# Kernel tuning notes

Measured on AMD Instinct MI355X. Metric: run time of the kernel, lower is better.

## Reference

```python
import jax, jax.numpy as jnp
import numpy as np

EMBED_DIM = 1024
NUM_HEADS = 16
PROJ_DIM = EMBED_DIM // NUM_HEADS


def setup_inputs() -> dict:
    key = jax.random.key(0)
    ks = jax.random.split(key, 11)
    B, S, D = 2, 2048, EMBED_DIM
    scale = 1.0 / np.sqrt(D)
    inp = {
        'q': jax.random.normal(ks[0], (B, S, D), jnp.float32),
        'k': jax.random.normal(ks[1], (B, S, D), jnp.float32),
        'v': jax.random.normal(ks[2], (B, S, D), jnp.float32),
        'Wq': jax.random.normal(ks[3], (D, D), jnp.float32) * scale,
        'bq': jnp.zeros((D,), jnp.float32),
        'Wk': jax.random.normal(ks[4], (D, D), jnp.float32) * scale,
        'bk': jnp.zeros((D,), jnp.float32),
        'Wv': jax.random.normal(ks[5], (D, D), jnp.float32) * scale,
        'bv': jnp.zeros((D,), jnp.float32),
        'Wo': jax.random.normal(ks[6], (D, D), jnp.float32) * scale,
        'bo': jnp.zeros((D,), jnp.float32),
        'use_causal_mask': 1,
    }
    return inp


def _split_heads(x, B):
    # [B, S, D] -> [B, H, S, Pd]
    return x.reshape(B, -1, NUM_HEADS, PROJ_DIM).transpose(0, 2, 1, 3)


def reference(q, k, v, Wq, bq, Wk, bk, Wv, bv, Wo, bo, use_causal_mask):
    B, S, D = q.shape
    qh = _split_heads(q @ Wq + bq, B)
    kh = _split_heads(k @ Wk + bk, B)
    vh = _split_heads(v @ Wv + bv, B)
    # scaled dot-product attention; scores [B, H, S, S]
    logits = jnp.einsum('bhqd,bhkd->bhqk', qh, kh) / jnp.sqrt(
        jnp.asarray(PROJ_DIM, jnp.float32))
    if use_causal_mask:
        # faithful to source: logits += log(tril * 1e-9 + 1e-9)
        tril = jnp.tril(jnp.ones((S, S), dtype=logits.dtype))
        logits = logits + jnp.log(tril * 1e-9 + 1e-9)
    attn = jax.nn.softmax(logits, axis=-1)
    out = jnp.einsum('bhqk,bhkd->bhqd', attn, vh)
    out = out.transpose(0, 2, 1, 3).reshape(B, S, D)
    return out @ Wo + bo
```

## Files before the change

### kernel.cpp

```cpp
#include <hip/hip_runtime.h>
#include <hip/hip_bf16.h>
#include <stdint.h>

#define EMBED 1024
#define NH    16
#define PD    64
#define BATCH 2
#define SEQ   2048

typedef unsigned short u16;
typedef __attribute__((ext_vector_type(8))) short bf16x8;
typedef __attribute__((ext_vector_type(4))) float f32x4;

#define WAITALL() __builtin_amdgcn_s_waitcnt(0)

__device__ __forceinline__ float b2f(u16 x) {
  unsigned u = ((unsigned)x) << 16;
  return __builtin_bit_cast(float, u);
}
__device__ __forceinline__ u16 f2b(float x) {
  unsigned u = __builtin_bit_cast(unsigned, x);
  u += 0x7fffu + ((u >> 16) & 1u);
  return (u16)(u >> 16);
}
__device__ __forceinline__ float loadIn(const void* p, size_t i, int isf32) {
  return isf32 ? ((const float*)p)[i] : b2f(((const u16*)p)[i]);
}
__device__ __forceinline__ void async16(const void* g, void* l) {
  __builtin_amdgcn_global_load_lds((const __attribute__((address_space(1))) void*)g,
                                   (__attribute__((address_space(3))) void*)l,
                                   16, 0, 0);
}
__device__ __forceinline__ int swz(int row, int col) {
  return row * 64 + (col ^ ((row & 7) << 3));
}

__global__ void detect(const unsigned* q, int* flag) {
  if (threadIdx.x == 0) {
    int conc = 0;
    for (int i = 0; i < 64; i++) {
      unsigned lo = q[i] & 0xffffu;
      unsigned e = (lo >> 7) & 0xffu;
      if (e >= 110 && e <= 135) conc++;
    }
    *flag = (conc < 32) ? 1 : 0;
  }
}

__global__ __launch_bounds__(256) void conv_qkv(const void* q, const void* k,
                                                const void* v, u16* qb, u16* kb,
                                                u16* vb, const int* flag) {
  const int isf32 = flag[0];
  size_t i = ((size_t)blockIdx.x * 256 + threadIdx.x) * 8;
  const void* src = (blockIdx.y == 0) ? q : (blockIdx.y == 1) ? k : v;
  u16* dst = (blockIdx.y == 0) ? qb : (blockIdx.y == 1) ? kb : vb;
  u16 tmp[8];
  if (isf32) {
    const float* s = (const float*)src + i;
    float4 a = *(const float4*)s;
    float4 b = *(const float4*)(s + 4);
    tmp[0] = f2b(a.x); tmp[1] = f2b(a.y); tmp[2] = f2b(a.z); tmp[3] = f2b(a.w);
    tmp[4] = f2b(b.x); tmp[5] = f2b(b.y); tmp[6] = f2b(b.z); tmp[7] = f2b(b.w);
  } else {
    const uint4 r = *(const uint4*)((const u16*)src + i);
    *(uint4*)tmp = r;
  }
  *(uint4*)(dst + i) = *(uint4*)tmp;
}

__global__ __launch_bounds__(256) void conv_w(const void* Wq, const void* Wk,
                                              const void* Wv, const void* Wo,
                                              u16* out, const int* flag) {
  const int isf32 = flag[0];
  const void* W = (blockIdx.z == 0) ? Wq : (blockIdx.z == 1) ? Wk
                : (blockIdx.z == 2) ? Wv : Wo;
  u16* WT = out + (size_t)blockIdx.z * EMBED * EMBED;
  __shared__ float sh[64][65];
  int r0 = blockIdx.y * 64, c0 = blockIdx.x * 64;
  int col = threadIdx.x & 63;
  int rb  = threadIdx.x >> 6;
#pragma unroll
  for (int i = 0; i < 16; i++) {
    int row = i * 4 + rb;
    sh[row][col] = loadIn(W, (size_t)(r0 + row) * EMBED + c0 + col, isf32);
  }
  __syncthreads();
#pragma unroll
  for (int i = 0; i < 16; i++) {
    int row = i * 4 + rb;
    WT[(size_t)(c0 + row) * EMBED + r0 + col] = f2b(sh[col][row]);
  }
}

__device__ __forceinline__ void gemm_core(const u16* __restrict__ A,
                                          const u16* __restrict__ Bt,
                                          int tm, int tn, u16* lds,
                                          f32x4 acc[4][4]) {
  const int tid = threadIdx.x;
  const int lane = tid & 63;
  const int wv = tid >> 6;
  const int wm = (wv >> 1) * 64, wn = (wv & 1) * 64;
  const int l15 = lane & 15, quad = lane >> 4;
  const int rb = (lane & 7) << 3;
  u16* As = lds;
  u16* Bs = lds + 128 * 64;
  f32x4 z = {0.f, 0.f, 0.f, 0.f};
#pragma unroll
  for (int i = 0; i < 4; i++)
#pragma unroll
    for (int j = 0; j < 4; j++) acc[i][j] = z;

  for (int kt = 0; kt < EMBED; kt += 64) {
#pragma unroll
    for (int i = 0; i < 4; i++) {
      int c = i * 256 + tid;
      int row = c >> 3;
      int col = ((c & 7) << 3) ^ ((row & 7) << 3);
      async16(A + (size_t)(tm + row) * EMBED + kt + col, As + c * 8);
      async16(Bt + (size_t)(tn + row) * EMBED + kt + col, Bs + c * 8);
    }
    WAITALL();
    __syncthreads();
#pragma unroll
    for (int ks = 0; ks < 64; ks += 32) {
      int ko = (ks + quad * 8) ^ rb;
      bf16x8 af[4], bf[4];
#pragma unroll
      for (int mt = 0; mt < 4; mt++)
        af[mt] = *(const bf16x8*)(As + (wm + mt * 16 + l15) * 64 + ko);
#pragma unroll
      for (int nt = 0; nt < 4; nt++)
        bf[nt] = *(const bf16x8*)(Bs + (wn + nt * 16 + l15) * 64 + ko);
#pragma unroll
      for (int mt = 0; mt < 4; mt++)
#pragma unroll
        for (int nt = 0; nt < 4; nt++)
          acc[mt][nt] = __builtin_amdgcn_mfma_f32_16x16x32_bf16(
              af[mt], bf[nt], acc[mt][nt], 0, 0, 0);
    }
    WAITALL();
    __syncthreads();
  }
}

__global__ __launch_bounds__(256) void qkv_gemm(
    const u16* qb, const u16* kb, const u16* vb, const u16* wts,
    const void* bq, const void* bk, const void* bv,
    u16* Qh, u16* Kh, u16* Vt, const int* flag) {
  __shared__ __align__(16) u16 lds[2 * 128 * 64];
  const int isf32 = flag[0];
  int z = blockIdx.z;
  const u16* A = (z == 0) ? qb : (z == 1) ? kb : vb;
  const u16* Bt = wts + (size_t)z * EMBED * EMBED;
  const void* bias = (z == 0) ? bq : (z == 1) ? bk : bv;
  int tm = blockIdx.y * 128, tn = blockIdx.x * 128;
  f32x4 acc[4][4];
  gemm_core(A, Bt, tm, tn, lds, acc);

  int lane = threadIdx.x & 63, wv = threadIdx.x >> 6;
  int wm = (wv >> 1) * 64, wn = (wv & 1) * 64;
  int rbase = tm + wm + ((lane >> 4) << 2);
  int cbase = tn + wn + (lane & 15);
  if (z < 2) {
    u16* dst = (z == 0) ? Qh : Kh;
#pragma unroll
    for (int mt = 0; mt < 4; mt++)
#pragma unroll
      for (int nt = 0; nt < 4; nt++) {
        int col = cbase + nt * 16;
        float bv_ = loadIn(bias, col, isf32);
        int h = col >> 6, p = col & 63;
#pragma unroll
        for (int j = 0; j < 4; j++) {
          int row = rbase + mt * 16 + j;
          int b = row >> 11, s = row & 2047;
          dst[(((size_t)(b * NH + h) * SEQ) + s) * PD + p] =
              f2b(acc[mt][nt][j] + bv_);
        }
      }
  } else {
#pragma unroll
    for (int mt = 0; mt < 4; mt++)
#pragma unroll
      for (int nt = 0; nt < 4; nt++) {
        int col = cbase + nt * 16;
        float bv_ = loadIn(bias, col, isf32);
        int h = col >> 6, p = col & 63;
        int row0 = rbase + mt * 16;
        int b = row0 >> 11, s0 = row0 & 2047;
        ushort4 pk;
        pk.x = f2b(acc[mt][nt][0] + bv_);
        pk.y = f2b(acc[mt][nt][1] + bv_);
        pk.z = f2b(acc[mt][nt][2] + bv_);
        pk.w = f2b(acc[mt][nt][3] + bv_);
        *(ushort4*)(Vt + ((size_t)(b * NH + h) * PD + p) * SEQ + s0) = pk;
      }
  }
}

__global__ __launch_bounds__(256) void attn(const u16* __restrict__ Qh,
                                            const u16* __restrict__ Kh,
                                            const u16* __restrict__ Vt,
                                            u16* __restrict__ O,
                                            const int* __restrict__ maskflag) {
  __shared__ __align__(16) u16 Qs[128 * 64];
  __shared__ __align__(16) u16 Ks[64 * 64];
  __shared__ __align__(16) u16 Vs[64 * 64];
  __shared__ __align__(16) u16 Ps[128 * 64];
  const int bh = blockIdx.y;
  const int qt = blockIdx.x * 128;
  const int tid = threadIdx.x, lane = tid & 63, wv = tid >> 6;
  const int l15 = lane & 15, quad = lane >> 4;
  const int rb = (lane & 7) << 3;
  const size_t head = (size_t)bh * SEQ * PD;
  const bool causal = (maskflag[0] != 0);
  const float C = 0.18033688011112042f;

#pragma unroll
  for (int i = 0; i < 4; i++) {
    int c = i * 256 + tid;
    int row = c >> 3;
    int col = ((c & 7) << 3) ^ ((row & 7) << 3);
    async16(Qh + head + (size_t)(qt + row) * PD + col, Qs + c * 8);
  }

  float lacc[2][4];
  f32x4 oacc[2][4];
  f32x4 z4 = {0.f, 0.f, 0.f, 0.f};
#pragma unroll
  for (int mt = 0; mt < 2; mt++)
#pragma unroll
    for (int j = 0; j < 4; j++) lacc[mt][j] = 0.f;
#pragma unroll
  for (int mt = 0; mt < 2; mt++)
#pragma unroll
    for (int nt = 0; nt < 4; nt++) oacc[mt][nt] = z4;

  const int rowq = qt + wv * 32 + (quad << 2);

  for (int t = 0; t < SEQ / 64; t++) {
    const int k0 = t * 64;
#pragma unroll
    for (int i = 0; i < 2; i++) {
      int c = i * 256 + tid;
      int row = c >> 3;
      int col = ((c & 7) << 3) ^ ((row & 7) << 3);
      async16(Kh + head + (size_t)(k0 + row) * PD + col, Ks + c * 8);
      async16(Vt + head + (size_t)row * SEQ + k0 + col, Vs + c * 8);
    }
    WAITALL();
    __syncthreads();

    f32x4 s[2][4];
#pragma unroll
    for (int mt = 0; mt < 2; mt++)
#pragma unroll
      for (int nt = 0; nt < 4; nt++) s[mt][nt] = z4;
#pragma unroll
    for (int ks = 0; ks < 64; ks += 32) {
      int ko = (ks + quad * 8) ^ rb;
      bf16x8 aq[2];
      aq[0] = *(const bf16x8*)(Qs + (wv * 32 + l15) * 64 + ko);
      aq[1] = *(const bf16x8*)(Qs + (wv * 32 + 16 + l15) * 64 + ko);
#pragma unroll
      for (int nt = 0; nt < 4; nt++) {
        bf16x8 bk8 = *(const bf16x8*)(Ks + (nt * 16 + l15) * 64 + ko);
        s[0][nt] = __builtin_amdgcn_mfma_f32_16x16x32_bf16(aq[0], bk8, s[0][nt], 0, 0, 0);
        s[1][nt] = __builtin_amdgcn_mfma_f32_16x16x32_bf16(aq[1], bk8, s[1][nt], 0, 0, 0);
      }
    }

    const int mode = !causal ? 0 : (k0 > qt + 127 ? 2 : (k0 + 63 <= qt ? 0 : 1));
    const float ub = (mode == 2) ? -17.f : -16.f;
#pragma unroll
    for (int mt = 0; mt < 2; mt++) {
      const int row = rowq + mt * 16;
      const int prow = wv * 32 + mt * 16 + (quad << 2);
#pragma unroll
      for (int nt = 0; nt < 4; nt++) {
        const int col = k0 + nt * 16 + l15;
        const int pcol = nt * 16 + l15;
#pragma unroll
        for (int j = 0; j < 4; j++) {
          float bias = ub;
          if (mode == 1 && col > row + j) bias = -17.f;
          float p = exp2f(fmaf(s[mt][nt][j], C, bias));
          lacc[mt][j] += p;
          Ps[(prow + j) * 64 + (pcol ^ (((prow + j) & 7) << 3))] = f2b(p);
        }
      }
    }

#pragma unroll
    for (int ks = 0; ks < 64; ks += 32) {
      int ko = (ks + quad * 8) ^ rb;
      bf16x8 ap[2];
      ap[0] = *(const bf16x8*)(Ps + (wv * 32 + l15) * 64 + ko);
      ap[1] = *(const bf16x8*)(Ps + (wv * 32 + 16 + l15) * 64 + ko);
#pragma unroll
      for (int nt = 0; nt < 4; nt++) {
        bf16x8 bv8 = *(const bf16x8*)(Vs + (nt * 16 + l15) * 64 + ko);
        oacc[0][nt] = __builtin_amdgcn_mfma_f32_16x16x32_bf16(ap[0], bv8, oacc[0][nt], 0, 0, 0);
        oacc[1][nt] = __builtin_amdgcn_mfma_f32_16x16x32_bf16(ap[1], bv8, oacc[1][nt], 0, 0, 0);
      }
    }
    WAITALL();
    __syncthreads();
  }

#pragma unroll
  for (int off = 1; off < 16; off <<= 1)
#pragma unroll
    for (int mt = 0; mt < 2; mt++)
#pragma unroll
      for (int j = 0; j < 4; j++)
        lacc[mt][j] += __shfl_xor(lacc[mt][j], off, 64);

  const int b = bh >> 4, h = bh & 15;
#pragma unroll
  for (int mt = 0; mt < 2; mt++) {
#pragma unroll
    for (int j = 0; j < 4; j++) {
      float inv = 1.f / lacc[mt][j];
      int qrow = qt + wv * 32 + mt * 16 + (quad << 2) + j;
      size_t base = ((size_t)b * SEQ + qrow) * EMBED + h * PD;
#pragma unroll
      for (int nt = 0; nt < 4; nt++) {
        int p = nt * 16 + l15;
        O[base + p] = f2b(oacc[mt][nt][j] * inv);
      }
    }
  }
}

__global__ __launch_bounds__(256) void out_gemm(const u16* __restrict__ Ob,
                                                const u16* __restrict__ WoT,
                                                const void* __restrict__ bo,
                                                void* __restrict__ out,
                                                const int* __restrict__ flag) {
  __shared__ __align__(16) u16 lds[2 * 128 * 64];
  const int isf32 = flag[0];
  int tm = blockIdx.y * 128, tn = blockIdx.x * 128;
  f32x4 acc[4][4];
  gemm_core(Ob, WoT, tm, tn, lds, acc);
  int lane = threadIdx.x & 63, wv = threadIdx.x >> 6;
  int wm = (wv >> 1) * 64, wn = (wv & 1) * 64;
  int rbase = tm + wm + ((lane >> 4) << 2);
  int cbase = tn + wn + (lane & 15);
#pragma unroll
  for (int mt = 0; mt < 4; mt++)
#pragma unroll
    for (int nt = 0; nt < 4; nt++) {
      int col = cbase + nt * 16;
      float bv_ = loadIn(bo, col, isf32);
#pragma unroll
      for (int j = 0; j < 4; j++) {
        int row = rbase + mt * 16 + j;
        float val = acc[mt][nt][j] + bv_;
        size_t off = (size_t)row * EMBED + col;
        if (isf32) ((float*)out)[off] = val;
        else       ((u16*)out)[off]   = f2b(val);
      }
    }
}

extern "C" void kernel_launch(void* const* d_in, const int* in_sizes, int n_in,
                              void* d_out, int out_size, void* d_ws, size_t ws_size,
                              hipStream_t stream) {
  const void* q  = d_in[0];
  const void* k  = d_in[1];
  const void* v  = d_in[2];
  const void* Wq = d_in[3];
  const void* bq = d_in[4];
  const void* Wk = d_in[5];
  const void* bk = d_in[6];
  const void* Wv = d_in[7];
  const void* bv = d_in[8];
  const void* Wo = d_in[9];
  const void* bo = d_in[10];
  const int* msk = (const int*)d_in[11];

  char* ws = (char*)d_ws;
  int*  flag  = (int*)ws;
  u16*  qb    = (u16*)(ws + 64);
  u16*  kb    = qb + (size_t)4194304;
  u16*  vb    = kb + (size_t)4194304;
  u16*  WT    = vb + (size_t)4194304;
  u16*  Qh    = WT + (size_t)4194304;
  u16*  Kh    = Qh + (size_t)4194304;
  u16*  Vt    = Kh + (size_t)4194304;
  u16*  Ob    = Vt + (size_t)4194304;

  detect<<<1, 64, 0, stream>>>((const unsigned*)q, flag);
  conv_qkv<<<dim3(2048, 3), 256, 0, stream>>>(q, k, v, qb, kb, vb, flag);
  conv_w<<<dim3(16, 16, 4), 256, 0, stream>>>(Wq, Wk, Wv, Wo, WT, flag);
  qkv_gemm<<<dim3(8, 32, 3), 256, 0, stream>>>(qb, kb, vb, WT, bq, bk, bv,
                                               Qh, Kh, Vt, flag);
  attn<<<dim3(16, 32), 256, 0, stream>>>(Qh, Kh, Vt, Ob, msk);
  out_gemm<<<dim3(8, 32), 256, 0, stream>>>(Ob, WT + (size_t)3 * 1048576,
                                            bo, d_out, flag);
}
```

Before: 309.6 us.

## Keep attention probabilities in registers via transposed S=K·Q MFMA layout

Computes the score tile transposed (K as the A operand, Q as B) so each lane holds the probabilities for one query row across consecutive keys. Those values are packed to bf16 in registers and fed straight into the P·V MFMA as the B operand, which removes the Ps shared-memory staging buffer and its writes and reads. V fragments are now gathered with two 8-byte LDS reads per tile, row sums need only two cross-lane shuffles, and outputs are written as 8-byte vectors. The detect kernel is also changed to a wave ballot. The cost is split V reads and possible bank conflicts on them.

```diff
diff --git a/kernel.cpp b/kernel.cpp
--- a/kernel.cpp
+++ b/kernel.cpp
@@ -31,20 +31,14 @@
                                    (__attribute__((address_space(3))) void*)l,
                                    16, 0, 0);
 }
-__device__ __forceinline__ int swz(int row, int col) {
-  return row * 64 + (col ^ ((row & 7) << 3));
-}
 
 __global__ void detect(const unsigned* q, int* flag) {
-  if (threadIdx.x == 0) {
-    int conc = 0;
-    for (int i = 0; i < 64; i++) {
-      unsigned lo = q[i] & 0xffffu;
-      unsigned e = (lo >> 7) & 0xffu;
-      if (e >= 110 && e <= 135) conc++;
-    }
-    *flag = (conc < 32) ? 1 : 0;
-  }
+  int lane = threadIdx.x;
+  unsigned lo = q[lane] & 0xffffu;
+  unsigned e = (lo >> 7) & 0xffu;
+  int pred = (e >= 110 && e <= 135);
+  unsigned long long m = __ballot(pred);
+  if (lane == 0) flag[0] = (__popcll(m) < 32) ? 1 : 0;
 }
 
 __global__ __launch_bounds__(256) void conv_qkv(const void* q, const void* k,
@@ -101,7 +95,7 @@
   const int wv = tid >> 6;
   const int wm = (wv >> 1) * 64, wn = (wv & 1) * 64;
   const int l15 = lane & 15, quad = lane >> 4;
-  const int rb = (lane & 7) << 3;
+  const int rbx = (lane & 7) << 3;
   u16* As = lds;
   u16* Bs = lds + 128 * 64;
   f32x4 z = {0.f, 0.f, 0.f, 0.f};
@@ -123,7 +117,7 @@
     __syncthreads();
 #pragma unroll
     for (int ks = 0; ks < 64; ks += 32) {
-      int ko = (ks + quad * 8) ^ rb;
+      int ko = (ks + quad * 8) ^ rbx;
       bf16x8 af[4], bf[4];
 #pragma unroll
       for (int mt = 0; mt < 4; mt++)
@@ -206,12 +200,11 @@
   __shared__ __align__(16) u16 Qs[128 * 64];
   __shared__ __align__(16) u16 Ks[64 * 64];
   __shared__ __align__(16) u16 Vs[64 * 64];
-  __shared__ __align__(16) u16 Ps[128 * 64];
   const int bh = blockIdx.y;
   const int qt = blockIdx.x * 128;
   const int tid = threadIdx.x, lane = tid & 63, wv = tid >> 6;
   const int l15 = lane & 15, quad = lane >> 4;
-  const int rb = (lane & 7) << 3;
+  const int rbx = (lane & 7) << 3;
   const size_t head = (size_t)bh * SEQ * PD;
   const bool causal = (maskflag[0] != 0);
   const float C = 0.18033688011112042f;
@@ -224,19 +217,15 @@
     async16(Qh + head + (size_t)(qt + row) * PD + col, Qs + c * 8);
   }
 
-  float lacc[2][4];
-  f32x4 oacc[2][4];
+  float lacc[2] = {0.f, 0.f};
+  f32x4 oacc[4][2];
   f32x4 z4 = {0.f, 0.f, 0.f, 0.f};
 #pragma unroll
-  for (int mt = 0; mt < 2; mt++)
-#pragma unroll
-    for (int j = 0; j < 4; j++) lacc[mt][j] = 0.f;
-#pragma unroll
-  for (int mt = 0; mt < 2; mt++)
-#pragma unroll
-    for (int nt = 0; nt < 4; nt++) oacc[mt][nt] = z4;
-
-  const int rowq = qt + wv * 32 + (quad << 2);
+  for (int mt = 0; mt < 4; mt++)
+#pragma unroll
+    for (int n = 0; n < 2; n++) oacc[mt][n] = z4;
+
+  const int rowq = qt + wv * 32;
 
   for (int t = 0; t < SEQ / 64; t++) {
     const int k0 = t * 64;
@@ -251,57 +240,70 @@
     WAITALL();
     __syncthreads();
 
-    f32x4 s[2][4];
-#pragma unroll
-    for (int mt = 0; mt < 2; mt++)
-#pragma unroll
-      for (int nt = 0; nt < 4; nt++) s[mt][nt] = z4;
+    f32x4 st[4][2];
+#pragma unroll
+    for (int kt = 0; kt < 4; kt++)
+#pragma unroll
+      for (int n = 0; n < 2; n++) st[kt][n] = z4;
 #pragma unroll
     for (int ks = 0; ks < 64; ks += 32) {
-      int ko = (ks + quad * 8) ^ rb;
-      bf16x8 aq[2];
-      aq[0] = *(const bf16x8*)(Qs + (wv * 32 + l15) * 64 + ko);
-      aq[1] = *(const bf16x8*)(Qs + (wv * 32 + 16 + l15) * 64 + ko);
-#pragma unroll
-      for (int nt = 0; nt < 4; nt++) {
-        bf16x8 bk8 = *(const bf16x8*)(Ks + (nt * 16 + l15) * 64 + ko);
-        s[0][nt] = __builtin_amdgcn_mfma_f32_16x16x32_bf16(aq[0], bk8, s[0][nt], 0, 0, 0);
-        s[1][nt] = __builtin_amdgcn_mfma_f32_16x16x32_bf16(aq[1], bk8, s[1][nt], 0, 0, 0);
+      int ko = (ks + quad * 8) ^ rbx;
+      bf16x8 qf[2];
+      qf[0] = *(const bf16x8*)(Qs + (wv * 32 + l15) * 64 + ko);
+      qf[1] = *(const bf16x8*)(Qs + (wv * 32 + 16 + l15) * 64 + ko);
+#pragma unroll
+      for (int kt = 0; kt < 4; kt++) {
+        bf16x8 kf = *(const bf16x8*)(Ks + (kt * 16 + l15) * 64 + ko);
+        st[kt][0] = __builtin_amdgcn_mfma_f32_16x16x32_bf16(kf, qf[0], st[kt][0], 0, 0, 0);
+        st[kt][1] = __builtin_amdgcn_mfma_f32_16x16x32_bf16(kf, qf[1], st[kt][1], 0, 0, 0);
       }
     }
 
     const int mode = !causal ? 0 : (k0 > qt + 127 ? 2 : (k0 + 63 <= qt ? 0 : 1));
     const float ub = (mode == 2) ? -17.f : -16.f;
-#pragma unroll
-    for (int mt = 0; mt < 2; mt++) {
-      const int row = rowq + mt * 16;
-      const int prow = wv * 32 + mt * 16 + (quad << 2);
-#pragma unroll
-      for (int nt = 0; nt < 4; nt++) {
-        const int col = k0 + nt * 16 + l15;
-        const int pcol = nt * 16 + l15;
-#pragma unroll
-        for (int j = 0; j < 4; j++) {
+    unsigned pw[2][2][4];
+#pragma unroll
+    for (int kt = 0; kt < 4; kt++) {
+#pragma unroll
+      for (int n = 0; n < 2; n++) {
+        const int qrow = rowq + n * 16 + l15;
+        float p[4];
+#pragma unroll
+        for (int r = 0; r < 4; r++) {
           float bias = ub;
-          if (mode == 1 && col > row + j) bias = -17.f;
-          float p = exp2f(fmaf(s[mt][nt][j], C, bias));
-          lacc[mt][j] += p;
-          Ps[(prow + j) * 64 + (pcol ^ (((prow + j) & 7) << 3))] = f2b(p);
+          if (mode == 1) {
+            int kappa = k0 + kt * 16 + 4 * quad + r;
+            bias = (kappa > qrow) ? -17.f : -16.f;
+          }
+          p[r] = exp2f(fmaf(st[kt][n][r], C, bias));
+          lacc[n] += p[r];
         }
-      }
-    }
-
-#pragma unroll
-    for (int ks = 0; ks < 64; ks += 32) {
-      int ko = (ks + quad * 8) ^ rb;
-      bf16x8 ap[2];
-      ap[0] = *(const bf16x8*)(Ps + (wv * 32 + l15) * 64 + ko);
-      ap[1] = *(const bf16x8*)(Ps + (wv * 32 + 16 + l15) * 64 + ko);
-#pragma unroll
-      for (int nt = 0; nt < 4; nt++) {
-        bf16x8 bv8 = *(const bf16x8*)(Vs + (nt * 16 + l15) * 64 + ko);
-        oacc[0][nt] = __builtin_amdgcn_mfma_f32_16x16x32_bf16(ap[0], bv8, oacc[0][nt], 0, 0, 0);
-        oacc[1][nt] = __builtin_amdgcn_mfma_f32_16x16x32_bf16(ap[1], bv8, oacc[1][nt], 0, 0, 0);
+        pw[kt >> 1][n][(kt & 1) * 2 + 0] =
+            (unsigned)f2b(p[0]) | ((unsigned)f2b(p[1]) << 16);
+        pw[kt >> 1][n][(kt & 1) * 2 + 1] =
+            (unsigned)f2b(p[2]) | ((unsigned)f2b(p[3]) << 16);
+      }
+    }
+
+#pragma unroll
+    for (int p = 0; p < 2; p++) {
+      bf16x8 pf[2];
+      pf[0] = __builtin_bit_cast(bf16x8,
+          (uint4){pw[p][0][0], pw[p][0][1], pw[p][0][2], pw[p][0][3]});
+      pf[1] = __builtin_bit_cast(bf16x8,
+          (uint4){pw[p][1][0], pw[p][1][1], pw[p][1][2], pw[p][1][3]});
+#pragma unroll
+      for (int mt = 0; mt < 4; mt++) {
+        int row = mt * 16 + l15;
+        int sz = (row & 7) << 3;
+        int c1 = (p * 32 + 4 * quad) ^ sz;
+        int c2 = (p * 32 + 16 + 4 * quad) ^ sz;
+        ushort4 a = *(const ushort4*)(Vs + row * 64 + c1);
+        ushort4 bb = *(const ushort4*)(Vs + row * 64 + c2);
+        bf16x8 vf = {(short)a.x, (short)a.y, (short)a.z, (short)a.w,
+                     (short)bb.x, (short)bb.y, (short)bb.z, (short)bb.w};
+        oacc[mt][0] = __builtin_amdgcn_mfma_f32_16x16x32_bf16(vf, pf[0], oacc[mt][0], 0, 0, 0);
+        oacc[mt][1] = __builtin_amdgcn_mfma_f32_16x16x32_bf16(vf, pf[1], oacc[mt][1], 0, 0, 0);
       }
     }
     WAITALL();
@@ -309,26 +311,25 @@
   }
 
 #pragma unroll
-  for (int off = 1; off < 16; off <<= 1)
-#pragma unroll
-    for (int mt = 0; mt < 2; mt++)
-#pragma unroll
-      for (int j = 0; j < 4; j++)
-        lacc[mt][j] += __shfl_xor(lacc[mt][j], off, 64);
+  for (int n = 0; n < 2; n++) {
+    lacc[n] += __shfl_xor(lacc[n], 16, 64);
+    lacc[n] += __shfl_xor(lacc[n], 32, 64);
+  }
+  float inv[2] = {1.f / lacc[0], 1.f / lacc[1]};
 
   const int b = bh >> 4, h = bh & 15;
 #pragma unroll
-  for (int mt = 0; mt < 2; mt++) {
-#pragma unroll
-    for (int j = 0; j < 4; j++) {
-      float inv = 1.f / lacc[mt][j];
-      int qrow = qt + wv * 32 + mt * 16 + (quad << 2) + j;
-      size_t base = ((size_t)b * SEQ + qrow) * EMBED + h * PD;
-#pragma unroll
-      for (int nt = 0; nt < 4; nt++) {
-        int p = nt * 16 + l15;
-        O[base + p] = f2b(oacc[mt][nt][j] * inv);
-      }
+  for (int mt = 0; mt < 4; mt++) {
+#pragma unroll
+    for (int n = 0; n < 2; n++) {
+      int qrow = rowq + n * 16 + l15;
+      ushort4 w;
+      w.x = f2b(oacc[mt][n][0] * inv[n]);
+      w.y = f2b(oacc[mt][n][1] * inv[n]);
+      w.z = f2b(oacc[mt][n][2] * inv[n]);
+      w.w = f2b(oacc[mt][n][3] * inv[n]);
+      *(ushort4*)(O + ((size_t)b * SEQ + qrow) * EMBED + h * PD + mt * 16 +
+                  4 * quad) = w;
     }
   }
 }
```

New measurement: 302.9 us. -2.2%, faster.
